# Kernel tuning notes

Measured on AMD Instinct MI355X. Metric: run time of the kernel, lower is better.

The kernel has to match this reference:

```python
import jax, jax.numpy as jnp
import numpy as np

EMBED_DIM = 512
NUM_TYPES = 26
PER_TYPE = 128
NUM_CODES = NUM_TYPES * PER_TYPE
COMMIT = 0.25
TEMP = 0.07
N_TOKENS = 32768
SAMPLED_PER_TYPE = int(0.1 * PER_TYPE)  # 12


def _normalize(v, axis=-1):
    # matches F.normalize(p=2) with eps clamp
    return v / jnp.clip(jnp.linalg.norm(v, axis=axis, keepdims=True), 1e-12)


def setup_inputs() -> dict:
    key = jax.random.key(0)
    k1, k2, k3, k4 = jax.random.split(key, 4)
    x = jax.random.normal(k1, (N_TOKENS, EMBED_DIM), jnp.float32)
    Q = jax.random.randint(k2, (N_TOKENS,), 0, NUM_TYPES)
    initrange = 1.0 / EMBED_DIM
    emb = jax.random.uniform(k3, (NUM_CODES, EMBED_DIM), jnp.float32, -initrange, initrange)
    emb = _normalize(emb)  # mirrors _initialize_embeddings
    # deterministic stand-in for torch.randperm(num_per_type)[:sampled_num]
    perm = jax.random.permutation(k4, PER_TYPE)[:SAMPLED_PER_TYPE]
    sampled_indices = (jnp.arange(NUM_TYPES)[:, None] * PER_TYPE + perm[None, :]).reshape(-1)
    return {"x": x, "embeddings": emb, "Q": Q, "sampled_indices": sampled_indices}


def _code_indices(xn, embeddings, Q):
    # full [N, num_codes] squared distances, then select the 128-code slab of
    # each token's PTM type and argmin within it (equivalent to the per-type loop)
    d = ((xn ** 2).sum(-1, keepdims=True)
         + (embeddings ** 2).sum(-1)[None, :]
         - 2.0 * (xn @ embeddings.T))                      # [N, NUM_CODES]
    d = d.reshape(xn.shape[0], NUM_TYPES, PER_TYPE)
    d_sel = jnp.take_along_axis(d, Q[:, None, None], axis=1)[:, 0, :]  # [N, PER_TYPE]
    return jnp.argmin(d_sel, axis=1) + Q * PER_TYPE


def _uniform_loss(embeddings, sampled_indices):
    ne = _normalize(embeddings)
    se = ne[sampled_indices]                               # [S, D]
    sim = se @ se.T                                        # [S, S]
    labels = sampled_indices // PER_TYPE
    pos = (labels[None, :] == labels[:, None]).astype(jnp.float32)
    S = sampled_indices.shape[0]
    eye = jnp.eye(S, dtype=bool)
    sim = jnp.where(eye, -jnp.inf, sim)
    sim_exp = jnp.exp(sim / TEMP)                          # exp(-inf) = 0 kills diagonal
    sum_exp = sim_exp.sum(axis=1)
    pos_sum = (sim_exp * pos).sum(axis=1)
    return -jnp.log(pos_sum / sum_exp).mean()


def reference(x, embeddings, Q, sampled_indices):
    xn = _normalize(x)
    idx = _code_indices(xn, embeddings, Q)
    quantized = _normalize(embeddings[idx])
    q_latent = jnp.mean((quantized - jax.lax.stop_gradient(xn)) ** 2)
    e_latent = jnp.mean((xn - jax.lax.stop_gradient(quantized)) ** 2)
    loss = q_latent + COMMIT * e_latent
    uloss = _uniform_loss(embeddings, sampled_indices)
    out = xn + jax.lax.stop_gradient(quantized - xn)       # straight-through
    return out, loss, uloss, idx
```

## Files before the change

### kernel.cpp

```cpp
#include <hip/hip_runtime.h>
#include <math.h>

#define NTOK   32768
#define DIM    512
#define NTYPES 26
#define PT     128
#define NCODES 3328
#define NSAMP  312
#define INV_TEMP (1.0f / 0.07f)
#define MAXTILES 24

typedef __attribute__((ext_vector_type(8))) short short8;
typedef __attribute__((ext_vector_type(4))) float floatx4;

__device__ __forceinline__ void f2bf2(float f, unsigned short& h, unsigned short& l) {
    unsigned u = __float_as_uint(f);
    unsigned hb = (u + 0x7fffu + ((u >> 16) & 1u)) >> 16;
    h = (unsigned short)hb;
    float hf = __uint_as_float(hb << 16);
    float r = f - hf;
    unsigned u2 = __float_as_uint(r);
    l = (unsigned short)((u2 + 0x7fffu + ((u2 >> 16) & 1u)) >> 16);
}

__device__ __forceinline__ void cvt8(float4 a, float4 b, short8& h, short8& l) {
    union { short8 v; unsigned short u[8]; } H, L;
    f2bf2(a.x, H.u[0], L.u[0]); f2bf2(a.y, H.u[1], L.u[1]);
    f2bf2(a.z, H.u[2], L.u[2]); f2bf2(a.w, H.u[3], L.u[3]);
    f2bf2(b.x, H.u[4], L.u[4]); f2bf2(b.y, H.u[5], L.u[5]);
    f2bf2(b.z, H.u[6], L.u[6]); f2bf2(b.w, H.u[7], L.u[7]);
    h = H.v; l = L.v;
}

__device__ __forceinline__ void stage2(const unsigned short* g, unsigned short* l) {
    __builtin_amdgcn_global_load_lds((const __attribute__((address_space(1))) void*)g,
                                     (__attribute__((address_space(3))) void*)l, 16, 0, 0);
    __builtin_amdgcn_global_load_lds((const __attribute__((address_space(1))) void*)(g + 512),
                                     (__attribute__((address_space(3))) void*)(l + 512), 16, 0, 0);
}

__global__ __launch_bounds__(256) void k_pre(const float* __restrict__ emb,
                                             const int* __restrict__ Q,
                                             unsigned short* __restrict__ Bhg,
                                             unsigned short* __restrict__ Blg,
                                             float* __restrict__ sume,
                                             float* __restrict__ rinv,
                                             int* __restrict__ bhist,
                                             int* __restrict__ rankb,
                                             float* __restrict__ accg,
                                             int* __restrict__ donec) {
    int tid = threadIdx.x;
    int bid = blockIdx.x;
    if (bid < NCODES / 4) {
        if (bid == 0) {
            if (tid == 32) accg[0] = 0.0f;
            if (tid == 33) accg[1] = 0.0f;
            if (tid == 34) *donec = 0;
        }
        int wv = tid >> 6, lane = tid & 63;
        int c = bid * 4 + wv;
        const float4* row = (const float4*)(emb + (size_t)c * DIM);
        float4 v0 = row[lane * 2], v1 = row[lane * 2 + 1];
        float s = v0.x*v0.x + v0.y*v0.y + v0.z*v0.z + v0.w*v0.w
                + v1.x*v1.x + v1.y*v1.y + v1.z*v1.z + v1.w*v1.w;
        for (int m = 32; m; m >>= 1) s += __shfl_xor(s, m);
        if (lane == 0) {
            sume[c] = s;
            rinv[c] = 1.0f / fmaxf(sqrtf(s), 1e-12f);
        }
        union { short8 v; unsigned short u[8]; } hh, ll;
        f2bf2(v0.x, hh.u[0], ll.u[0]); f2bf2(v0.y, hh.u[1], ll.u[1]);
        f2bf2(v0.z, hh.u[2], ll.u[2]); f2bf2(v0.w, hh.u[3], ll.u[3]);
        f2bf2(v1.x, hh.u[4], ll.u[4]); f2bf2(v1.y, hh.u[5], ll.u[5]);
        f2bf2(v1.z, hh.u[6], ll.u[6]); f2bf2(v1.w, hh.u[7], ll.u[7]);
        int qq  = c >> 7;
        int n   = c & 127;
        int ni  = n >> 4, lcc = n & 15;
        int ks2 = lane >> 2, q4d = lane & 3;
        size_t dst = (size_t)qq * (PT * DIM)
                   + (size_t)(((ks2 * 8 + ni) * 64 + q4d * 16 + lcc) * 8);
        *(short8*)(Bhg + dst) = hh.v;
        *(short8*)(Blg + dst) = ll.v;
    } else {
        __shared__ int lbin[NTYPES];
        int hb = bid - NCODES / 4;
        if (tid < NTYPES) lbin[tid] = 0;
        __syncthreads();
        int t = hb * 256 + tid;
        int q = Q[t];
        int lr = atomicAdd(&lbin[q], 1);
        __syncthreads();
        if (tid < NTYPES) bhist[hb * 32 + tid] = lbin[tid];
        rankb[t] = lr;
    }
}

__global__ __launch_bounds__(256) void k_scat(const int* __restrict__ Q,
                                              const int* __restrict__ bhist,
                                              const int* __restrict__ rankb,
                                              const float* __restrict__ emb,
                                              const float* __restrict__ rinv,
                                              const int* __restrict__ samp,
                                              int* __restrict__ order,
                                              int* __restrict__ offsg,
                                              float* __restrict__ ne) {
    int b = blockIdx.x;
    int tid = threadIdx.x;
    if (b < NTOK / 256) {
        __shared__ int offs_s[NTYPES];
        __shared__ int base_s[NTYPES];
        if (tid < NTYPES) {
            int tot = 0, pre = 0;
            for (int bb = 0; bb < NTOK / 256; bb++) {
                int v = bhist[bb * 32 + tid];
                tot += v;
                if (bb < b) pre += v;
            }
            offs_s[tid] = tot;
            base_s[tid] = pre;
        }
        __syncthreads();
        if (tid == 0) {
            int a = 0;
            for (int t2 = 0; t2 < NTYPES; t2++) {
                int tt = offs_s[t2];
                offs_s[t2] = a;
                if (b == 0) offsg[t2] = a;
                a += tt;
            }
            if (b == 0) offsg[NTYPES] = a;
        }
        __syncthreads();
        int t = b * 256 + tid;
        int q = Q[t];
        order[offs_s[q] + base_s[q] + rankb[t]] = t;
    } else {
        int lane = tid & 63, wv = tid >> 6;
        int i = (b - NTOK / 256) * 4 + wv;
        int ci = samp[i];
        float rv = rinv[ci];
        const float4* er = (const float4*)(emb + (size_t)ci * DIM);
        float4 e0 = er[lane * 2], e1 = er[lane * 2 + 1];
        float4* nr = (float4*)(ne + (size_t)i * DIM);
        nr[lane * 2]     = make_float4(e0.x * rv, e0.y * rv, e0.z * rv, e0.w * rv);
        nr[lane * 2 + 1] = make_float4(e1.x * rv, e1.y * rv, e1.z * rv, e1.w * rv);
    }
}

#define KSTEP(S, NSTR, AC, AF, DOSTAGE)                                          \
  {                                                                              \
    __builtin_amdgcn_sched_barrier(0);                                           \
    asm volatile("s_waitcnt vmcnt(" NSTR ")" ::: "memory");                      \
    __builtin_amdgcn_s_barrier();                                                \
    __builtin_amdgcn_sched_barrier(0);                                           \
    if (DOSTAGE) {                                                               \
      stage2(bhg + ((S) + 2) * 4096 + stoff, &Bls[((S) + 2) % 3][0][ldoff]);     \
      stage2(blg + ((S) + 2) * 4096 + stoff, &Bls[((S) + 2) % 3][1][ldoff]);     \
      AF[0] = *(const float4*)(ap0 + ((S) + 2) * 32);                            \
      AF[1] = *(const float4*)(ap0 + ((S) + 2) * 32 + 4);                        \
      AF[2] = *(const float4*)(ap1 + ((S) + 2) * 32);                            \
      AF[3] = *(const float4*)(ap1 + ((S) + 2) * 32 + 4);                        \
    }                                                                            \
    __builtin_amdgcn_sched_barrier(0);                                           \
    {                                                                            \
      float4 r0a = AC[0], r0b = AC[1], r1a = AC[2], r1b = AC[3];                 \
      ps0 = fmaf(r0a.x, r0a.x, fmaf(r0a.y, r0a.y, fmaf(r0a.z, r0a.z, fmaf(r0a.w, r0a.w, ps0)))); \
      ps0 = fmaf(r0b.x, r0b.x, fmaf(r0b.y, r0b.y, fmaf(r0b.z, r0b.z, fmaf(r0b.w, r0b.w, ps0)))); \
      ps1 = fmaf(r1a.x, r1a.x, fmaf(r1a.y, r1a.y, fmaf(r1a.z, r1a.z, fmaf(r1a.w, r1a.w, ps1)))); \
      ps1 = fmaf(r1b.x, r1b.x, fmaf(r1b.y, r1b.y, fmaf(r1b.z, r1b.z, fmaf(r1b.w, r1b.w, ps1)))); \
      short8 ah0, al0, ah1, al1;                                                 \
      cvt8(r0a, r0b, ah0, al0);                                                  \
      cvt8(r1a, r1b, ah1, al1);                                                  \
      short8 bhf[4], blf[4];                                                     \
      _Pragma("unroll")                                                          \
      for (int ni = 0; ni < 4; ni++) {                                           \
        bhf[ni] = *(const short8*)&Bls[(S) % 3][0][(wn4 + ni) * 512 + lane8];    \
        blf[ni] = *(const short8*)&Bls[(S) % 3][1][(wn4 + ni) * 512 + lane8];    \
      }                                                                          \
      _Pragma("unroll")                                                          \
      for (int ni = 0; ni < 4; ni++) {                                           \
        acc[0][ni] = __builtin_amdgcn_mfma_f32_16x16x32_bf16(ah0, bhf[ni], acc[0][ni], 0, 0, 0); \
        acc[0][ni] = __builtin_amdgcn_mfma_f32_16x16x32_bf16(ah0, blf[ni], acc[0][ni], 0, 0, 0); \
        acc[0][ni] = __builtin_amdgcn_mfma_f32_16x16x32_bf16(al0, bhf[ni], acc[0][ni], 0, 0, 0); \
        acc[1][ni] = __builtin_amdgcn_mfma_f32_16x16x32_bf16(ah1, bhf[ni], acc[1][ni], 0, 0, 0); \
        acc[1][ni] = __builtin_amdgcn_mfma_f32_16x16x32_bf16(ah1, blf[ni], acc[1][ni], 0, 0, 0); \
        acc[1][ni] = __builtin_amdgcn_mfma_f32_16x16x32_bf16(al1, bhf[ni], acc[1][ni], 0, 0, 0); \
      }                                                                          \
    }                                                                            \
  }

__global__ __launch_bounds__(256, 3) void k_main(const float* __restrict__ x,
                                                 const unsigned short* __restrict__ Bhg,
                                                 const unsigned short* __restrict__ Blg,
                                                 const int* __restrict__ order,
                                                 const int* __restrict__ offsg,
                                                 const float* __restrict__ sume,
                                                 const float* __restrict__ rinv,
                                                 float* __restrict__ idxout,
                                                 float* __restrict__ accg) {
    int q = blockIdx.x;
    int tile = blockIdx.y;
    int base = offsg[q];
    int cnt = offsg[q + 1] - base;
    int tstart = tile * 64;
    if (tstart >= cnt) return;
    int nt = min(64, cnt - tstart);

    __shared__ unsigned short Bls[3][2][4096];
    __shared__ int   toks_s[64];
    __shared__ float sume_s[128];
    __shared__ float rinv_s[128];
    __shared__ float redv[64][2];
    __shared__ int   redi[64][2];

    int tid = threadIdx.x;
    int lane = tid & 63;
    int wv = tid >> 6;
    int wm = wv & 1, wn = wv >> 1;
    int lc = lane & 15, q4 = lane >> 4;
    int wn4 = wn * 4, lane8 = lane * 8;
    int stoff = wv * 1024 + lane8;
    int ldoff = wv * 1024;

    if (tid < 64) toks_s[tid] = order[base + tstart + min(tid, nt - 1)];
    if (tid < 128) {
        sume_s[tid] = sume[q * PT + tid];
        rinv_s[tid] = rinv[q * PT + tid];
    }

    int row0 = wm * 32 + lc;
    int tok0 = order[base + tstart + min(row0, nt - 1)];
    int tok1 = order[base + tstart + min(row0 + 16, nt - 1)];
    const float* ap0 = x + (size_t)tok0 * DIM + q4 * 8;
    const float* ap1 = x + (size_t)tok1 * DIM + q4 * 8;

    const unsigned short* bhg = Bhg + (size_t)q * (PT * DIM);
    const unsigned short* blg = Blg + (size_t)q * (PT * DIM);

    floatx4 acc[2][4];
#pragma unroll
    for (int mi = 0; mi < 2; mi++)
#pragma unroll
        for (int ni = 0; ni < 4; ni++)
            acc[mi][ni] = (floatx4){0.f, 0.f, 0.f, 0.f};
    float ps0 = 0.f, ps1 = 0.f;
    float4 Aa[4], Ab[4], Ac[4];

    stage2(bhg + stoff, &Bls[0][0][ldoff]);
    stage2(blg + stoff, &Bls[0][1][ldoff]);
    __builtin_amdgcn_sched_barrier(0);
    Aa[0] = *(const float4*)(ap0);      Aa[1] = *(const float4*)(ap0 + 4);
    Aa[2] = *(const float4*)(ap1);      Aa[3] = *(const float4*)(ap1 + 4);
    __builtin_amdgcn_sched_barrier(0);
    stage2(bhg + 4096 + stoff, &Bls[1][0][ldoff]);
    stage2(blg + 4096 + stoff, &Bls[1][1][ldoff]);
    __builtin_amdgcn_sched_barrier(0);
    Ab[0] = *(const float4*)(ap0 + 32); Ab[1] = *(const float4*)(ap0 + 36);
    Ab[2] = *(const float4*)(ap1 + 32); Ab[3] = *(const float4*)(ap1 + 36);

    KSTEP(0,  "8", Aa, Ac, 1)
    KSTEP(1,  "8", Ab, Aa, 1)
    KSTEP(2,  "8", Ac, Ab, 1)
    KSTEP(3,  "8", Aa, Ac, 1)
    KSTEP(4,  "8", Ab, Aa, 1)
    KSTEP(5,  "8", Ac, Ab, 1)
    KSTEP(6,  "8", Aa, Ac, 1)
    KSTEP(7,  "8", Ab, Aa, 1)
    KSTEP(8,  "8", Ac, Ab, 1)
    KSTEP(9,  "8", Aa, Ac, 1)
    KSTEP(10, "8", Ab, Aa, 1)
    KSTEP(11, "8", Ac, Ab, 1)
    KSTEP(12, "8", Aa, Ac, 1)
    KSTEP(13, "8", Ab, Aa, 1)
    KSTEP(14, "8", Ac, Ab, 0)
    KSTEP(15, "0", Aa, Ab, 0)

    ps0 += __shfl_xor(ps0, 16); ps0 += __shfl_xor(ps0, 32);
    ps1 += __shfl_xor(ps1, 16); ps1 += __shfl_xor(ps1, 32);
    float rn0 = 1.0f / fmaxf(sqrtf(ps0), 1e-12f);
    float rn1 = 1.0f / fmaxf(sqrtf(ps1), 1e-12f);

#pragma unroll
    for (int mi = 0; mi < 2; mi++) {
#pragma unroll
        for (int r = 0; r < 4; r++) {
            int rowrel = q4 * 4 + r;
            float rn = __shfl(mi == 0 ? rn0 : rn1, rowrel);
            float rn2v = -2.0f * rn;
            float bv = 1e30f; int bc = 0;
#pragma unroll
            for (int ni = 0; ni < 4; ni++) {
                int n = wn * 64 + ni * 16 + lc;
                float d = fmaf(rn2v, acc[mi][ni][r], sume_s[n]);
                if (d < bv) { bv = d; bc = n; }
            }
#pragma unroll
            for (int mk = 1; mk <= 8; mk <<= 1) {
                float ov = __shfl_xor(bv, mk);
                int oc = __shfl_xor(bc, mk);
                if (ov < bv || (ov == bv && oc < bc)) { bv = ov; bc = oc; }
            }
            int m = wm * 32 + mi * 16 + rowrel;
            if (lc == 0) { redv[m][wn] = bv; redi[m][wn] = bc; }
        }
    }
    __syncthreads();

    if (tid < 64) {
        float v0 = redv[tid][0], v1 = redv[tid][1];
        int c = (v1 < v0) ? redi[tid][1] : redi[tid][0];
        float bvv = fminf(v0, v1);
        float term = 0.0f;
        if (tid < nt) {
            idxout[toks_s[tid]] = (float)(q * PT + c);
            term = 2.0f - (sume_s[c] - bvv) * rinv_s[c];
        }
        for (int mk = 32; mk; mk >>= 1) term += __shfl_xor(term, mk);
        if (tid == 0) atomicAdd(&accg[0], term);
    }
}

__global__ __launch_bounds__(256) void k_out(const float* __restrict__ emb,
                                             const float* __restrict__ rinv,
                                             const float* __restrict__ idxf,
                                             float* __restrict__ outbuf) {
    int tid = threadIdx.x, lane = tid & 63, wv = tid >> 6;
    int tbase = blockIdx.x * 64 + wv * 16;
    int cL = 0; float rvL = 0.f;
    if (lane < 16) {
        cL = (int)idxf[tbase + lane];
        rvL = rinv[cL];
    }
    const float4* er = (const float4*)emb;
    int c0 = __shfl(cL, 0); float rv0 = __shfl(rvL, 0);
    float4 ea = er[(size_t)c0 * 128 + lane * 2];
    float4 eb = er[(size_t)c0 * 128 + lane * 2 + 1];
#pragma unroll
    for (int t = 0; t < 16; t++) {
        float4 ca = ea, cb = eb;
        float rv = rv0;
        if (t < 15) {
            int c1 = __shfl(cL, t + 1);
            rv0 = __shfl(rvL, t + 1);
            ea = er[(size_t)c1 * 128 + lane * 2];
            eb = er[(size_t)c1 * 128 + lane * 2 + 1];
        }
        float4* orow = (float4*)(outbuf + (size_t)(tbase + t) * DIM);
        orow[lane * 2]     = make_float4(ca.x * rv, ca.y * rv, ca.z * rv, ca.w * rv);
        orow[lane * 2 + 1] = make_float4(cb.x * rv, cb.y * rv, cb.z * rv, cb.w * rv);
    }
}

__global__ __launch_bounds__(256) void k_uloss(const float* __restrict__ ne,
                                               const int* __restrict__ samp,
                                               float* __restrict__ accg,
                                               int* __restrict__ donec,
                                               float* __restrict__ lossp) {
    __shared__ float rs[4], rp[4];
    int i = blockIdx.x;
    int tid = threadIdx.x;
    int lane = tid & 63, wv = tid >> 6;
    int labi = samp[i] >> 7;
    const float4* ri = (const float4*)(ne + (size_t)i * DIM);
    float4 e0 = ri[lane * 2], e1 = ri[lane * 2 + 1];
    float sE = 0.0f, pE = 0.0f;
    for (int j0 = wv; j0 < NSAMP; j0 += 16) {
        float d[4]; int lj[4]; bool val[4];
#pragma unroll
        for (int u = 0; u < 4; u++) {
            int j = j0 + u * 4;
            val[u] = (j < NSAMP) && (j != i);
            int js = val[u] ? j : 0;
            lj[u] = samp[js] >> 7;
            const float4* rj = (const float4*)(ne + (size_t)js * DIM);
            float4 f0 = rj[lane * 2], f1 = rj[lane * 2 + 1];
            d[u] = e0.x*f0.x + e0.y*f0.y + e0.z*f0.z + e0.w*f0.w
                 + e1.x*f1.x + e1.y*f1.y + e1.z*f1.z + e1.w*f1.w;
        }
#pragma unroll
        for (int mk = 32; mk; mk >>= 1)
#pragma unroll
            for (int u = 0; u < 4; u++) d[u] += __shfl_xor(d[u], mk);
#pragma unroll
        for (int u = 0; u < 4; u++) {
            float ex = val[u] ? expf(d[u] * INV_TEMP) : 0.0f;
            sE += ex;
            if (val[u] && lj[u] == labi) pE += ex;
        }
    }
    if (lane == 0) { rs[wv] = sE; rp[wv] = pE; }
    __syncthreads();
    if (tid == 0) {
        float S = rs[0] + rs[1] + rs[2] + rs[3];
        float P = rp[0] + rp[1] + rp[2] + rp[3];
        atomicAdd(&accg[1], logf(S) - logf(P));
        __threadfence();
        int old = atomicAdd(donec, 1);
        if (old == NSAMP - 1) {
            __threadfence();
            float a0 = atomicAdd(&accg[0], 0.0f);
            float a1 = atomicAdd(&accg[1], 0.0f);
            lossp[0] = (1.25f / ((float)NTOK * (float)DIM)) * a0;
            lossp[1] = a1 / (float)NSAMP;
        }
    }
}

extern "C" void kernel_launch(void* const* d_in, const int* in_sizes, int n_in,
                              void* d_out, int out_size, void* d_ws, size_t ws_size,
                              hipStream_t stream) {
    const float* x   = (const float*)d_in[0];
    const float* emb = (const float*)d_in[1];
    const int* Q     = (const int*)d_in[2];
    const int* samp  = (const int*)d_in[3];

    float* out    = (float*)d_out;
    float* lossp  = out + (size_t)NTOK * DIM;
    float* idxout = out + (size_t)NTOK * DIM + 2;

    unsigned short* Bhg = (unsigned short*)d_ws;
    unsigned short* Blg = Bhg + (size_t)NCODES * DIM;
    float* sume  = (float*)(Blg + (size_t)NCODES * DIM);
    float* rinv  = sume + NCODES;
    int* bhist   = (int*)(rinv + NCODES);
    int* rankb   = bhist + (NTOK / 256) * 32;
    int* offsg   = rankb + NTOK;
    int* order   = offsg + 32;
    float* ne    = (float*)(order + NTOK);
    float* accg  = ne + (size_t)NSAMP * DIM;
    int* donec   = (int*)(accg + 2);

    k_pre<<<NCODES / 4 + NTOK / 256, 256, 0, stream>>>(emb, Q, Bhg, Blg, sume, rinv,
                                                       bhist, rankb, accg, donec);
    k_scat<<<NTOK / 256 + NSAMP / 4, 256, 0, stream>>>(Q, bhist, rankb, emb, rinv,
                                                       samp, order, offsg, ne);
    dim3 gmain(NTYPES, MAXTILES);
    k_main<<<gmain, 256, 0, stream>>>(x, Bhg, Blg, order, offsg, sume, rinv,
                                      idxout, accg);
    k_out<<<NTOK / 64, 256, 0, stream>>>(emb, rinv, idxout, out);
    k_uloss<<<NSAMP, 256, 0, stream>>>(ne, samp, accg, donec, lossp);
}
```

Measured before the change: 204.8 us.

## Use 128-token tiles with 512-thread blocks and XCD-aware type mapping

The main distance kernel now processes 128 tokens per block with 8 waves instead of 64 tokens with 4 waves. Each staged codebook slab in LDS is therefore reused across twice as many tokens, and each wave issues half as many global-to-LDS loads. The grid is flattened so that each PTM type maps to one XCD (bid&7), which keeps that type's codebook traffic within one XCD's L2. The cost is fewer, larger blocks, about 270 active out of 384 launched, so wave-level load balance and occupancy may suffer. Launch bounds also change to 512 threads with 4 blocks per CU, which tightens the register budget.

```diff
diff --git a/kernel.cpp b/kernel.cpp
--- a/kernel.cpp
+++ b/kernel.cpp
@@ -8,7 +8,7 @@
 #define NCODES 3328
 #define NSAMP  312
 #define INV_TEMP (1.0f / 0.07f)
-#define MAXTILES 24
+#define TILES128 12
 
 typedef __attribute__((ext_vector_type(8))) short short8;
 typedef __attribute__((ext_vector_type(4))) float floatx4;
@@ -32,11 +32,13 @@
     h = H.v; l = L.v;
 }
 
-__device__ __forceinline__ void stage2(const unsigned short* g, unsigned short* l) {
+__device__ __forceinline__ void gll1(const unsigned short* g, unsigned short* l) {
     __builtin_amdgcn_global_load_lds((const __attribute__((address_space(1))) void*)g,
                                      (__attribute__((address_space(3))) void*)l, 16, 0, 0);
-    __builtin_amdgcn_global_load_lds((const __attribute__((address_space(1))) void*)(g + 512),
-                                     (__attribute__((address_space(3))) void*)(l + 512), 16, 0, 0);
+}
+__device__ __forceinline__ void stage2(const unsigned short* g, unsigned short* l) {
+    gll1(g, l);
+    gll1(g + 512, l + 512);
 }
 
 __global__ __launch_bounds__(256) void k_pre(const float* __restrict__ emb,
@@ -154,8 +156,8 @@
     __builtin_amdgcn_s_barrier();                                                \
     __builtin_amdgcn_sched_barrier(0);                                           \
     if (DOSTAGE) {                                                               \
-      stage2(bhg + ((S) + 2) * 4096 + stoff, &Bls[((S) + 2) % 3][0][ldoff]);     \
-      stage2(blg + ((S) + 2) * 4096 + stoff, &Bls[((S) + 2) % 3][1][ldoff]);     \
+      gll1(bhg + ((S) + 2) * 4096 + stoff, &Bls[((S) + 2) % 3][0][ldoff]);       \
+      gll1(blg + ((S) + 2) * 4096 + stoff, &Bls[((S) + 2) % 3][1][ldoff]);       \
       AF[0] = *(const float4*)(ap0 + ((S) + 2) * 32);                            \
       AF[1] = *(const float4*)(ap0 + ((S) + 2) * 32 + 4);                        \
       AF[2] = *(const float4*)(ap1 + ((S) + 2) * 32);                            \
@@ -189,7 +191,7 @@
     }                                                                            \
   }
 
-__global__ __launch_bounds__(256, 3) void k_main(const float* __restrict__ x,
+__global__ __launch_bounds__(512, 4) void k_main(const float* __restrict__ x,
                                                  const unsigned short* __restrict__ Bhg,
                                                  const unsigned short* __restrict__ Blg,
                                                  const int* __restrict__ order,
@@ -198,32 +200,37 @@
                                                  const float* __restrict__ rinv,
                                                  float* __restrict__ idxout,
                                                  float* __restrict__ accg) {
-    int q = blockIdx.x;
-    int tile = blockIdx.y;
+    int bid = blockIdx.x;
+    int xcd = bid & 7;
+    int j = bid >> 3;
+    int jt = j / TILES128;
+    int tile = j - jt * TILES128;
+    int q = xcd + 8 * jt;
+    if (q >= NTYPES) return;
     int base = offsg[q];
     int cnt = offsg[q + 1] - base;
-    int tstart = tile * 64;
+    int tstart = tile * 128;
     if (tstart >= cnt) return;
-    int nt = min(64, cnt - tstart);
+    int nt = min(128, cnt - tstart);
 
     __shared__ unsigned short Bls[3][2][4096];
-    __shared__ int   toks_s[64];
+    __shared__ int   toks_s[128];
     __shared__ float sume_s[128];
     __shared__ float rinv_s[128];
-    __shared__ float redv[64][2];
-    __shared__ int   redi[64][2];
+    __shared__ float redv[128][2];
+    __shared__ int   redi[128][2];
 
     int tid = threadIdx.x;
     int lane = tid & 63;
     int wv = tid >> 6;
-    int wm = wv & 1, wn = wv >> 1;
+    int wm = wv & 3, wn = wv >> 2;
     int lc = lane & 15, q4 = lane >> 4;
     int wn4 = wn * 4, lane8 = lane * 8;
-    int stoff = wv * 1024 + lane8;
-    int ldoff = wv * 1024;
-
-    if (tid < 64) toks_s[tid] = order[base + tstart + min(tid, nt - 1)];
+    int stoff = wv * 512 + lane8;
+    int ldoff = wv * 512;
+
     if (tid < 128) {
+        toks_s[tid] = order[base + tstart + min(tid, nt - 1)];
         sume_s[tid] = sume[q * PT + tid];
         rinv_s[tid] = rinv[q * PT + tid];
     }
@@ -246,33 +253,33 @@
     float ps0 = 0.f, ps1 = 0.f;
     float4 Aa[4], Ab[4], Ac[4];
 
-    stage2(bhg + stoff, &Bls[0][0][ldoff]);
-    stage2(blg + stoff, &Bls[0][1][ldoff]);
+    gll1(bhg + stoff, &Bls[0][0][ldoff]);
+    gll1(blg + stoff, &Bls[0][1][ldoff]);
     __builtin_amdgcn_sched_barrier(0);
     Aa[0] = *(const float4*)(ap0);      Aa[1] = *(const float4*)(ap0 + 4);
     Aa[2] = *(const float4*)(ap1);      Aa[3] = *(const float4*)(ap1 + 4);
     __builtin_amdgcn_sched_barrier(0);
-    stage2(bhg + 4096 + stoff, &Bls[1][0][ldoff]);
-    stage2(blg + 4096 + stoff, &Bls[1][1][ldoff]);
+    gll1(bhg + 4096 + stoff, &Bls[1][0][ldoff]);
+    gll1(blg + 4096 + stoff, &Bls[1][1][ldoff]);
     __builtin_amdgcn_sched_barrier(0);
     Ab[0] = *(const float4*)(ap0 + 32); Ab[1] = *(const float4*)(ap0 + 36);
     Ab[2] = *(const float4*)(ap1 + 32); Ab[3] = *(const float4*)(ap1 + 36);
 
-    KSTEP(0,  "8", Aa, Ac, 1)
-    KSTEP(1,  "8", Ab, Aa, 1)
-    KSTEP(2,  "8", Ac, Ab, 1)
-    KSTEP(3,  "8", Aa, Ac, 1)
-    KSTEP(4,  "8", Ab, Aa, 1)
-    KSTEP(5,  "8", Ac, Ab, 1)
-    KSTEP(6,  "8", Aa, Ac, 1)
-    KSTEP(7,  "8", Ab, Aa, 1)
-    KSTEP(8,  "8", Ac, Ab, 1)
-    KSTEP(9,  "8", Aa, Ac, 1)
-    KSTEP(10, "8", Ab, Aa, 1)
-    KSTEP(11, "8", Ac, Ab, 1)
-    KSTEP(12, "8", Aa, Ac, 1)
-    KSTEP(13, "8", Ab, Aa, 1)
-    KSTEP(14, "8", Ac, Ab, 0)
+    KSTEP(0,  "6", Aa, Ac, 1)
+    KSTEP(1,  "6", Ab, Aa, 1)
+    KSTEP(2,  "6", Ac, Ab, 1)
+    KSTEP(3,  "6", Aa, Ac, 1)
+    KSTEP(4,  "6", Ab, Aa, 1)
+    KSTEP(5,  "6", Ac, Ab, 1)
+    KSTEP(6,  "6", Aa, Ac, 1)
+    KSTEP(7,  "6", Ab, Aa, 1)
+    KSTEP(8,  "6", Ac, Ab, 1)
+    KSTEP(9,  "6", Aa, Ac, 1)
+    KSTEP(10, "6", Ab, Aa, 1)
+    KSTEP(11, "6", Ac, Ab, 1)
+    KSTEP(12, "6", Aa, Ac, 1)
+    KSTEP(13, "6", Ab, Aa, 1)
+    KSTEP(14, "6", Ac, Ab, 0)
     KSTEP(15, "0", Aa, Ab, 0)
 
     ps0 += __shfl_xor(ps0, 16); ps0 += __shfl_xor(ps0, 32);
@@ -306,7 +313,7 @@
     }
     __syncthreads();
 
-    if (tid < 64) {
+    if (tid < 128) {
         float v0 = redv[tid][0], v1 = redv[tid][1];
         int c = (v1 < v0) ? redi[tid][1] : redi[tid][0];
         float bvv = fminf(v0, v1);
@@ -316,7 +323,7 @@
             term = 2.0f - (sume_s[c] - bvv) * rinv_s[c];
         }
         for (int mk = 32; mk; mk >>= 1) term += __shfl_xor(term, mk);
-        if (tid == 0) atomicAdd(&accg[0], term);
+        if (lane == 0) atomicAdd(&accg[0], term);
     }
 }
 
@@ -434,9 +441,8 @@
                                                        bhist, rankb, accg, donec);
     k_scat<<<NTOK / 256 + NSAMP / 4, 256, 0, stream>>>(Q, bhist, rankb, emb, rinv,
                                                        samp, order, offsg, ne);
-    dim3 gmain(NTYPES, MAXTILES);
-    k_main<<<gmain, 256, 0, stream>>>(x, Bhg, Blg, order, offsg, sume, rinv,
-                                      idxout, accg);
+    k_main<<<8 * 4 * TILES128, 512, 0, stream>>>(x, Bhg, Blg, order, offsg, sume, rinv,
+                                                 idxout, accg);
     k_out<<<NTOK / 64, 256, 0, stream>>>(emb, rinv, idxout, out);
     k_uloss<<<NSAMP, 256, 0, stream>>>(ne, samp, accg, donec, lossp);
 }
```

After: 214.2 us. 4.6% more time.

## Repartition main-kernel warps to own 16 rows across all 128 codes

Applied to the files above, without the earlier changes.

Changes the per-wave tile from a 2x2 wave grid (32 rows x 64 codes each) to four waves that each own 16 token rows and all 128 codes. Each wave now loads and converts only one A row-slice, so the fp32 x loads and hi/lo bf16 splitting are no longer done twice per row. The argmin finishes within a wave, removing the cross-wave merge of partial minima. In exchange each wave reads twice as much B fragment data from LDS per k-step, which raises LDS traffic, and the vmcnt wait counts are adjusted to match the fewer outstanding global loads.

```diff
diff --git a/kernel.cpp b/kernel.cpp
--- a/kernel.cpp
+++ b/kernel.cpp
@@ -156,35 +156,30 @@
     if (DOSTAGE) {                                                               \
       stage2(bhg + ((S) + 2) * 4096 + stoff, &Bls[((S) + 2) % 3][0][ldoff]);     \
       stage2(blg + ((S) + 2) * 4096 + stoff, &Bls[((S) + 2) % 3][1][ldoff]);     \
-      AF[0] = *(const float4*)(ap0 + ((S) + 2) * 32);                            \
-      AF[1] = *(const float4*)(ap0 + ((S) + 2) * 32 + 4);                        \
-      AF[2] = *(const float4*)(ap1 + ((S) + 2) * 32);                            \
-      AF[3] = *(const float4*)(ap1 + ((S) + 2) * 32 + 4);                        \
+      AF[0] = *(const float4*)(ap + ((S) + 2) * 32);                             \
+      AF[1] = *(const float4*)(ap + ((S) + 2) * 32 + 4);                         \
     }                                                                            \
     __builtin_amdgcn_sched_barrier(0);                                           \
     {                                                                            \
-      float4 r0a = AC[0], r0b = AC[1], r1a = AC[2], r1b = AC[3];                 \
-      ps0 = fmaf(r0a.x, r0a.x, fmaf(r0a.y, r0a.y, fmaf(r0a.z, r0a.z, fmaf(r0a.w, r0a.w, ps0)))); \
-      ps0 = fmaf(r0b.x, r0b.x, fmaf(r0b.y, r0b.y, fmaf(r0b.z, r0b.z, fmaf(r0b.w, r0b.w, ps0)))); \
-      ps1 = fmaf(r1a.x, r1a.x, fmaf(r1a.y, r1a.y, fmaf(r1a.z, r1a.z, fmaf(r1a.w, r1a.w, ps1)))); \
-      ps1 = fmaf(r1b.x, r1b.x, fmaf(r1b.y, r1b.y, fmaf(r1b.z, r1b.z, fmaf(r1b.w, r1b.w, ps1)))); \
-      short8 ah0, al0, ah1, al1;                                                 \
-      cvt8(r0a, r0b, ah0, al0);                                                  \
-      cvt8(r1a, r1b, ah1, al1);                                                  \
-      short8 bhf[4], blf[4];                                                     \
+      float4 a0 = AC[0], a1 = AC[1];                                             \
+      ps = fmaf(a0.x, a0.x, fmaf(a0.y, a0.y, fmaf(a0.z, a0.z, fmaf(a0.w, a0.w, ps)))); \
+      ps = fmaf(a1.x, a1.x, fmaf(a1.y, a1.y, fmaf(a1.z, a1.z, fmaf(a1.w, a1.w, ps)))); \
+      short8 ah, al;                                                             \
+      cvt8(a0, a1, ah, al);                                                      \
       _Pragma("unroll")                                                          \
-      for (int ni = 0; ni < 4; ni++) {                                           \
-        bhf[ni] = *(const short8*)&Bls[(S) % 3][0][(wn4 + ni) * 512 + lane8];    \
-        blf[ni] = *(const short8*)&Bls[(S) % 3][1][(wn4 + ni) * 512 + lane8];    \
-      }                                                                          \
-      _Pragma("unroll")                                                          \
-      for (int ni = 0; ni < 4; ni++) {                                           \
-        acc[0][ni] = __builtin_amdgcn_mfma_f32_16x16x32_bf16(ah0, bhf[ni], acc[0][ni], 0, 0, 0); \
-        acc[0][ni] = __builtin_amdgcn_mfma_f32_16x16x32_bf16(ah0, blf[ni], acc[0][ni], 0, 0, 0); \
-        acc[0][ni] = __builtin_amdgcn_mfma_f32_16x16x32_bf16(al0, bhf[ni], acc[0][ni], 0, 0, 0); \
-        acc[1][ni] = __builtin_amdgcn_mfma_f32_16x16x32_bf16(ah1, bhf[ni], acc[1][ni], 0, 0, 0); \
-        acc[1][ni] = __builtin_amdgcn_mfma_f32_16x16x32_bf16(ah1, blf[ni], acc[1][ni], 0, 0, 0); \
-        acc[1][ni] = __builtin_amdgcn_mfma_f32_16x16x32_bf16(al1, bhf[ni], acc[1][ni], 0, 0, 0); \
+      for (int h = 0; h < 2; h++) {                                              \
+        short8 bhf[4], blf[4];                                                   \
+        _Pragma("unroll")                                                        \
+        for (int j = 0; j < 4; j++) {                                            \
+          bhf[j] = *(const short8*)&Bls[(S) % 3][0][(h * 4 + j) * 512 + lane8];  \
+          blf[j] = *(const short8*)&Bls[(S) % 3][1][(h * 4 + j) * 512 + lane8];  \
+        }                                                                        \
+        _Pragma("unroll")                                                        \
+        for (int j = 0; j < 4; j++) {                                            \
+          acc[h * 4 + j] = __builtin_amdgcn_mfma_f32_16x16x32_bf16(ah, bhf[j], acc[h * 4 + j], 0, 0, 0); \
+          acc[h * 4 + j] = __builtin_amdgcn_mfma_f32_16x16x32_bf16(ah, blf[j], acc[h * 4 + j], 0, 0, 0); \
+          acc[h * 4 + j] = __builtin_amdgcn_mfma_f32_16x16x32_bf16(al, bhf[j], acc[h * 4 + j], 0, 0, 0); \
+        }                                                                        \
       }                                                                          \
     }                                                                            \
   }
@@ -210,15 +205,14 @@
     __shared__ int   toks_s[64];
     __shared__ float sume_s[128];
     __shared__ float rinv_s[128];
-    __shared__ float redv[64][2];
-    __shared__ int   redi[64][2];
+    __shared__ float redv[64];
+    __shared__ int   redi[64];
 
     int tid = threadIdx.x;
     int lane = tid & 63;
     int wv = tid >> 6;
-    int wm = wv & 1, wn = wv >> 1;
     int lc = lane & 15, q4 = lane >> 4;
-    int wn4 = wn * 4, lane8 = lane * 8;
+    int lane8 = lane * 8;
     int stoff = wv * 1024 + lane8;
     int ldoff = wv * 1024;
 
@@ -228,88 +222,75 @@
         rinv_s[tid] = rinv[q * PT + tid];
     }
 
-    int row0 = wm * 32 + lc;
-    int tok0 = order[base + tstart + min(row0, nt - 1)];
-    int tok1 = order[base + tstart + min(row0 + 16, nt - 1)];
-    const float* ap0 = x + (size_t)tok0 * DIM + q4 * 8;
-    const float* ap1 = x + (size_t)tok1 * DIM + q4 * 8;
+    int rowA = wv * 16 + lc;
+    int tokA = order[base + tstart + min(rowA, nt - 1)];
+    const float* ap = x + (size_t)tokA * DIM + q4 * 8;
 
     const unsigned short* bhg = Bhg + (size_t)q * (PT * DIM);
     const unsigned short* blg = Blg + (size_t)q * (PT * DIM);
 
-    floatx4 acc[2][4];
-#pragma unroll
-    for (int mi = 0; mi < 2; mi++)
-#pragma unroll
-        for (int ni = 0; ni < 4; ni++)
-            acc[mi][ni] = (floatx4){0.f, 0.f, 0.f, 0.f};
-    float ps0 = 0.f, ps1 = 0.f;
-    float4 Aa[4], Ab[4], Ac[4];
+    floatx4 acc[8];
+#pragma unroll
+    for (int ni = 0; ni < 8; ni++) acc[ni] = (floatx4){0.f, 0.f, 0.f, 0.f};
+    float ps = 0.f;
+    float4 Aa[2], Ab[2], Ac[2];
 
     stage2(bhg + stoff, &Bls[0][0][ldoff]);
     stage2(blg + stoff, &Bls[0][1][ldoff]);
     __builtin_amdgcn_sched_barrier(0);
-    Aa[0] = *(const float4*)(ap0);      Aa[1] = *(const float4*)(ap0 + 4);
-    Aa[2] = *(const float4*)(ap1);      Aa[3] = *(const float4*)(ap1 + 4);
+    Aa[0] = *(const float4*)(ap);       Aa[1] = *(const float4*)(ap + 4);
     __builtin_amdgcn_sched_barrier(0);
     stage2(bhg + 4096 + stoff, &Bls[1][0][ldoff]);
     stage2(blg + 4096 + stoff, &Bls[1][1][ldoff]);
     __builtin_amdgcn_sched_barrier(0);
-    Ab[0] = *(const float4*)(ap0 + 32); Ab[1] = *(const float4*)(ap0 + 36);
-    Ab[2] = *(const float4*)(ap1 + 32); Ab[3] = *(const float4*)(ap1 + 36);
-
-    KSTEP(0,  "8", Aa, Ac, 1)
-    KSTEP(1,  "8", Ab, Aa, 1)
-    KSTEP(2,  "8", Ac, Ab, 1)
-    KSTEP(3,  "8", Aa, Ac, 1)
-    KSTEP(4,  "8", Ab, Aa, 1)
-    KSTEP(5,  "8", Ac, Ab, 1)
-    KSTEP(6,  "8", Aa, Ac, 1)
-    KSTEP(7,  "8", Ab, Aa, 1)
-    KSTEP(8,  "8", Ac, Ab, 1)
-    KSTEP(9,  "8", Aa, Ac, 1)
-    KSTEP(10, "8", Ab, Aa, 1)
-    KSTEP(11, "8", Ac, Ab, 1)
-    KSTEP(12, "8", Aa, Ac, 1)
-    KSTEP(13, "8", Ab, Aa, 1)
-    KSTEP(14, "8", Ac, Ab, 0)
+    Ab[0] = *(const float4*)(ap + 32);  Ab[1] = *(const float4*)(ap + 36);
+
+    KSTEP(0,  "6", Aa, Ac, 1)
+    KSTEP(1,  "6", Ab, Aa, 1)
+    KSTEP(2,  "6", Ac, Ab, 1)
+    KSTEP(3,  "6", Aa, Ac, 1)
+    KSTEP(4,  "6", Ab, Aa, 1)
+    KSTEP(5,  "6", Ac, Ab, 1)
+    KSTEP(6,  "6", Aa, Ac, 1)
+    KSTEP(7,  "6", Ab, Aa, 1)
+    KSTEP(8,  "6", Ac, Ab, 1)
+    KSTEP(9,  "6", Aa, Ac, 1)
+    KSTEP(10, "6", Ab, Aa, 1)
+    KSTEP(11, "6", Ac, Ab, 1)
+    KSTEP(12, "6", Aa, Ac, 1)
+    KSTEP(13, "6", Ab, Aa, 1)
+    KSTEP(14, "6", Ac, Ab, 0)
     KSTEP(15, "0", Aa, Ab, 0)
 
-    ps0 += __shfl_xor(ps0, 16); ps0 += __shfl_xor(ps0, 32);
-    ps1 += __shfl_xor(ps1, 16); ps1 += __shfl_xor(ps1, 32);
-    float rn0 = 1.0f / fmaxf(sqrtf(ps0), 1e-12f);
-    float rn1 = 1.0f / fmaxf(sqrtf(ps1), 1e-12f);
-
-#pragma unroll
-    for (int mi = 0; mi < 2; mi++) {
-#pragma unroll
-        for (int r = 0; r < 4; r++) {
-            int rowrel = q4 * 4 + r;
-            float rn = __shfl(mi == 0 ? rn0 : rn1, rowrel);
-            float rn2v = -2.0f * rn;
-            float bv = 1e30f; int bc = 0;
-#pragma unroll
-            for (int ni = 0; ni < 4; ni++) {
-                int n = wn * 64 + ni * 16 + lc;
-                float d = fmaf(rn2v, acc[mi][ni][r], sume_s[n]);
-                if (d < bv) { bv = d; bc = n; }
-            }
-#pragma unroll
-            for (int mk = 1; mk <= 8; mk <<= 1) {
-                float ov = __shfl_xor(bv, mk);
-                int oc = __shfl_xor(bc, mk);
-                if (ov < bv || (ov == bv && oc < bc)) { bv = ov; bc = oc; }
-            }
-            int m = wm * 32 + mi * 16 + rowrel;
-            if (lc == 0) { redv[m][wn] = bv; redi[m][wn] = bc; }
-        }
+    ps += __shfl_xor(ps, 16);
+    ps += __shfl_xor(ps, 32);
+    float rnv = 1.0f / fmaxf(sqrtf(ps), 1e-12f);
+
+#pragma unroll
+    for (int r = 0; r < 4; r++) {
+        int rowrel = q4 * 4 + r;
+        float rn2v = -2.0f * __shfl(rnv, rowrel);
+        float bv = 1e30f; int bc = 0;
+#pragma unroll
+        for (int ni = 0; ni < 8; ni++) {
+            int n = ni * 16 + lc;
+            float d = fmaf(rn2v, acc[ni][r], sume_s[n]);
+            if (d < bv) { bv = d; bc = n; }
+        }
+#pragma unroll
+        for (int mk = 1; mk <= 8; mk <<= 1) {
+            float ov = __shfl_xor(bv, mk);
+            int oc = __shfl_xor(bc, mk);
+            if (ov < bv || (ov == bv && oc < bc)) { bv = ov; bc = oc; }
+        }
+        int m = wv * 16 + rowrel;
+        if (lc == 0) { redv[m] = bv; redi[m] = bc; }
     }
     __syncthreads();
 
     if (tid < 64) {
-        float v0 = redv[tid][0], v1 = redv[tid][1];
-        int c = (v1 < v0) ? redi[tid][1] : redi[tid][0];
-        float bvv = fminf(v0, v1);
+        int c = redi[tid];
+        float bvv = redv[tid];
         float term = 0.0f;
         if (tid < nt) {
             idxout[toks_s[tid]] = (float)(q * PT + c);
```

Result: faster. 197.6 us (-3.5%).
